# Optimization experiments

Measured on AMD Instinct MI355X. Metric: run time of the kernel, lower is better.

Reference implementation:

```python
import jax, jax.numpy as jnp
import numpy as np

SINKHORN_ITERS = 8
TEMPERATURE = 1.0
EPS = 1e-6


def sinkhorn(t):
    # log-domain Sinkhorn normalization, matching torch: log(clamp(t, min=eps)) / temp
    t = jnp.log(jnp.clip(t, EPS)) / TEMPERATURE
    for _ in range(SINKHORN_ITERS):
        t = t - jax.nn.logsumexp(t, axis=-2, keepdims=True)  # over tokens n
        t = t - jax.nn.logsumexp(t, axis=-1, keepdims=True)  # over experts e
    return jnp.exp(t)


def setup_inputs() -> dict:
    key = jax.random.key(0)
    k1, k2, k3 = jax.random.split(key, 3)
    B, N, D, E = 4, 4096, 1024, 8
    x = jax.random.normal(k1, (B, N, D), dtype=jnp.float32)
    gate_w = jax.random.normal(k2, (D, E), dtype=jnp.float32) * (D ** -0.5)
    experts = jax.random.normal(k3, (E, D, D), dtype=jnp.float32) * (D ** -0.5)
    return {"x": x, "gate_w": gate_w, "experts": experts}


def reference(x, gate_w, experts):
    B, N, D = x.shape
    E = gate_w.shape[-1]
    M = N // E  # tokens per expert

    gate_logits = jnp.einsum('bnd,de->bne', x, gate_w)
    competitive_gates = sinkhorn(gate_logits)  # b n e

    # topk along token dim (-2): transpose to (b,e,n), top_k along last axis
    vals, idx = jax.lax.top_k(jnp.swapaxes(competitive_gates, -1, -2), M)  # b e m
    gate_values = jnp.swapaxes(vals, -1, -2)   # b m e
    routed_indices = jnp.swapaxes(idx, -1, -2)  # b m e (int32)

    b_idx = jnp.arange(B)[:, None, None]  # (b,1,1)
    routed = x[b_idx, routed_indices]     # b m e d
    routed = jnp.transpose(routed, (2, 0, 1, 3))  # e b m d

    outputs = jnp.einsum('ebmd,edf->ebmf', routed, experts)  # e b m d
    outputs = outputs * jnp.transpose(gate_values, (2, 0, 1))[..., None]  # * (e b m 1)

    vals_bmed = jnp.transpose(outputs, (1, 2, 0, 3))  # b m e d
    routed_back = jnp.zeros_like(x).at[b_idx, routed_indices].set(vals_bmed)
    return routed_back
```

## Files before the change

kernel.cpp:

```cpp
#include <hip/hip_runtime.h>
#include <hip/hip_bf16.h>
#include <stdint.h>

typedef short s16x8 __attribute__((ext_vector_type(8)));
typedef float f32x4 __attribute__((ext_vector_type(4)));
typedef unsigned short u16;
typedef unsigned int u32;
typedef unsigned long long u64;

__device__ __forceinline__ float bf2f(u16 v){
  union { u32 u; float f; } c; c.u = ((u32)v) << 16; return c.f;
}

__device__ __forceinline__ u16 f2bf(float f){
  u32 u = __float_as_uint(f);
  u32 r = (u + 0x7FFFu + ((u >> 16) & 1u)) >> 16;
  return (u16)r;
}

__device__ __forceinline__ uint4 pack8(float4 a, float4 b){
  union { uint4 v; u16 s[8]; } o;
  o.s[0]=f2bf(a.x); o.s[1]=f2bf(a.y); o.s[2]=f2bf(a.z); o.s[3]=f2bf(a.w);
  o.s[4]=f2bf(b.x); o.s[5]=f2bf(b.y); o.s[6]=f2bf(b.z); o.s[7]=f2bf(b.w);
  return o.v;
}

__global__ __launch_bounds__(64) void k_detect(const u32* __restrict__ x, int* __restrict__ flag){
  int lane = threadIdx.x;
  int cnt = 0;
  for (int i = lane; i < 4096; i += 64){
    u32 w = x[i];
    int ex = (w >> 7) & 0xFF;
    cnt += (ex >= 140) ? 1 : 0;
  }
  #pragma unroll
  for (int off = 32; off; off >>= 1) cnt += __shfl_xor(cnt, off, 64);
  if (lane == 0) *flag = (cnt > 256) ? 1 : 0;
}

__global__ __launch_bounds__(1024) void k_logits_cvt(const void* __restrict__ xv,
                                                     const void* __restrict__ gwv,
                                                     const int* __restrict__ flag,
                                                     u16* __restrict__ xb,
                                                     float* __restrict__ gates,
                                                     int mode){
  __shared__ float4 gw_swz[2048];
  __shared__ float  wacc[16][8];
  int is_f32 = *flag;
  int tid = threadIdx.x;

  {
    int r = tid;
    float g0,g1,g2,g3,g4,g5,g6,g7;
    if (is_f32){
      const float* gw = (const float*)gwv + ((size_t)r << 3);
      float4 u = *(const float4*)gw;
      float4 v = *(const float4*)(gw + 4);
      g0=u.x; g1=u.y; g2=u.z; g3=u.w; g4=v.x; g5=v.y; g6=v.z; g7=v.w;
    } else {
      union { uint4 v; u16 s[8]; } wu;
      wu.v = *(const uint4*)((const u16*)gwv + ((size_t)r << 3));
      g0=bf2f(wu.s[0]); g1=bf2f(wu.s[1]); g2=bf2f(wu.s[2]); g3=bf2f(wu.s[3]);
      g4=bf2f(wu.s[4]); g5=bf2f(wu.s[5]); g6=bf2f(wu.s[6]); g7=bf2f(wu.s[7]);
    }
    int p = r >> 3, j = r & 7;
    gw_swz[(p << 4) + (((j << 1)    ) ^ (p & 15))] = make_float4(g0,g1,g2,g3);
    gw_swz[(p << 4) + (((j << 1) | 1) ^ (p & 15))] = make_float4(g4,g5,g6,g7);
  }

  int tl = tid >> 7, pos = tid & 127;
  size_t base = ((((size_t)blockIdx.x << 3) + tl) << 10) + ((size_t)pos << 3);
  float xf[8];
  if (is_f32){
    const float* xr = (const float*)xv + base;
    float4 u = *(const float4*)xr;
    float4 v = *(const float4*)(xr + 4);
    xf[0]=u.x; xf[1]=u.y; xf[2]=u.z; xf[3]=u.w;
    xf[4]=v.x; xf[5]=v.y; xf[6]=v.z; xf[7]=v.w;
    if (mode) *(uint4*)(xb + base) = pack8(u, v);
  } else {
    uint4 raw = *(const uint4*)((const u16*)xv + base);
    union { uint4 v; u16 s[8]; } xu; xu.v = raw;
    #pragma unroll
    for (int k = 0; k < 8; k++) xf[k] = bf2f(xu.s[k]);
    if (mode) *(uint4*)(xb + base) = raw;
  }
  __syncthreads();

  float a0=0,a1=0,a2=0,a3=0,a4=0,a5=0,a6=0,a7=0;
  #pragma unroll
  for (int j = 0; j < 8; j++){
    float4 wA = gw_swz[(pos << 4) + (((j << 1)    ) ^ (pos & 15))];
    float4 wB = gw_swz[(pos << 4) + (((j << 1) | 1) ^ (pos & 15))];
    float xv8 = xf[j];
    a0 += xv8*wA.x; a1 += xv8*wA.y; a2 += xv8*wA.z; a3 += xv8*wA.w;
    a4 += xv8*wB.x; a5 += xv8*wB.y; a6 += xv8*wB.z; a7 += xv8*wB.w;
  }
  #pragma unroll
  for (int off = 32; off; off >>= 1){
    a0 += __shfl_xor(a0, off, 64); a1 += __shfl_xor(a1, off, 64);
    a2 += __shfl_xor(a2, off, 64); a3 += __shfl_xor(a3, off, 64);
    a4 += __shfl_xor(a4, off, 64); a5 += __shfl_xor(a5, off, 64);
    a6 += __shfl_xor(a6, off, 64); a7 += __shfl_xor(a7, off, 64);
  }
  int wave = tid >> 6, lane = tid & 63;
  if (lane == 0){
    wacc[wave][0]=a0; wacc[wave][1]=a1; wacc[wave][2]=a2; wacc[wave][3]=a3;
    wacc[wave][4]=a4; wacc[wave][5]=a5; wacc[wave][6]=a6; wacc[wave][7]=a7;
  }
  __syncthreads();
  if (tid < 64){
    int tt = tid >> 3, e = tid & 7;
    float v = wacc[(tt << 1)][e] + wacc[(tt << 1) | 1][e];
    gates[((((size_t)blockIdx.x << 3) + tt) << 3) + e] = v;
  }
}

__global__ __launch_bounds__(1024) void k_sink_cover(float* __restrict__ gates,
                                                     const void* __restrict__ Wv,
                                                     const int* __restrict__ flag,
                                                     u16* __restrict__ WT,
                                                     uint4* __restrict__ out,
                                                     int out_size, int mode){
  __shared__ __align__(16) char smem[36864];
  int bx = blockIdx.x;
  int tid = threadIdx.x;

  if (bx < 4){
    float* wred = (float*)smem;
    float* lbc  = wred + 128;
    int wave = tid >> 6, lane = tid & 63;
    float* gb = gates + ((size_t)bx << 15);
    float4 va[4], vb[4];
    #pragma unroll
    for (int q = 0; q < 4; q++){
      float* gp = gb + (((q << 10) + tid) << 3);
      float4 a = *(const float4*)gp;
      float4 b = *(const float4*)(gp + 4);
      a.x=fmaxf(a.x,1e-6f); a.y=fmaxf(a.y,1e-6f); a.z=fmaxf(a.z,1e-6f); a.w=fmaxf(a.w,1e-6f);
      b.x=fmaxf(b.x,1e-6f); b.y=fmaxf(b.y,1e-6f); b.z=fmaxf(b.z,1e-6f); b.w=fmaxf(b.w,1e-6f);
      va[q]=a; vb[q]=b;
    }
    for (int it = 0; it < 8; it++){
      float s0 = ((va[0].x+va[1].x)+(va[2].x+va[3].x));
      float s1 = ((va[0].y+va[1].y)+(va[2].y+va[3].y));
      float s2 = ((va[0].z+va[1].z)+(va[2].z+va[3].z));
      float s3 = ((va[0].w+va[1].w)+(va[2].w+va[3].w));
      float s4 = ((vb[0].x+vb[1].x)+(vb[2].x+vb[3].x));
      float s5 = ((vb[0].y+vb[1].y)+(vb[2].y+vb[3].y));
      float s6 = ((vb[0].z+vb[1].z)+(vb[2].z+vb[3].z));
      float s7 = ((vb[0].w+vb[1].w)+(vb[2].w+vb[3].w));
      #pragma unroll
      for (int off = 32; off; off >>= 1){
        s0 += __shfl_xor(s0, off, 64); s1 += __shfl_xor(s1, off, 64);
        s2 += __shfl_xor(s2, off, 64); s3 += __shfl_xor(s3, off, 64);
        s4 += __shfl_xor(s4, off, 64); s5 += __shfl_xor(s5, off, 64);
        s6 += __shfl_xor(s6, off, 64); s7 += __shfl_xor(s7, off, 64);
      }
      if (lane == 0){
        wred[(wave<<3)+0]=s0; wred[(wave<<3)+1]=s1; wred[(wave<<3)+2]=s2; wred[(wave<<3)+3]=s3;
        wred[(wave<<3)+4]=s4; wred[(wave<<3)+5]=s5; wred[(wave<<3)+6]=s6; wred[(wave<<3)+7]=s7;
      }
      __syncthreads();
      if (tid < 8){
        float S = 0.f;
        #pragma unroll
        for (int w2 = 0; w2 < 16; w2++) S += wred[(w2 << 3) + tid];
        lbc[tid] = 1.0f / S;
      }
      __syncthreads();
      float i0=lbc[0], i1=lbc[1], i2=lbc[2], i3=lbc[3];
      float i4=lbc[4], i5=lbc[5], i6=lbc[6], i7=lbc[7];
      #pragma unroll
      for (int q = 0; q < 4; q++){
        float4 a = va[q], b = vb[q];
        a.x*=i0; a.y*=i1; a.z*=i2; a.w*=i3;
        b.x*=i4; b.y*=i5; b.z*=i6; b.w*=i7;
        float rs = ((a.x+a.y)+(a.z+a.w)) + ((b.x+b.y)+(b.z+b.w));
        float ir = 1.0f / rs;
        a.x*=ir; a.y*=ir; a.z*=ir; a.w*=ir;
        b.x*=ir; b.y*=ir; b.z*=ir; b.w*=ir;
        va[q]=a; vb[q]=b;
      }
    }
    #pragma unroll
    for (int q = 0; q < 4; q++){
      float* gp = gb + (((q << 10) + tid) << 3);
      *(float4*)gp = va[q];
      *(float4*)(gp + 4) = vb[q];
    }
    return;
  }

  if (mode == 0){
    int is_f32 = *flag;
    int rb = bx - 4;
    size_t words = (size_t)out_size >> (is_f32 ? 0 : 1);
    size_t n4 = words >> 2;
    size_t i = (size_t)rb * 1024 + tid;
    uint4 z = make_uint4(0, 0, 0, 0);
    for (; i < n4; i += (size_t)512 * 1024) out[i] = z;
    return;
  }

  if (bx < 516){
    int is_f32 = *flag;
    int rb = bx - 4;
    int sub = tid >> 8;
    int t = tid & 255;
    int g = (rb << 2) + sub;
    int e = g >> 8, t2 = g & 255;
    int td = (t2 >> 4) << 6, tf = (t2 & 15) << 6;
    u16 (*tile)[72] = (u16(*)[72])(smem + (size_t)sub * (64 * 72 * 2));
    #pragma unroll
    for (int i = 0; i < 2; i++){
      int id = t + (i << 8);
      int row = id >> 3, c8 = id & 7;
      size_t src = ((size_t)(e*1024 + td + row))*1024 + tf + (c8 << 3);
      uint4 v;
      if (is_f32){
        const float* wf = (const float*)Wv;
        v = pack8(*(const float4*)(wf + src), *(const float4*)(wf + src + 4));
      } else {
        v = *(const uint4*)((const u16*)Wv + src);
      }
      *(uint4*)&tile[row][c8 << 3] = v;
    }
    __syncthreads();
    #pragma unroll
    for (int i = 0; i < 2; i++){
      int id = t + (i << 8);
      int frow = id >> 3, c8 = id & 7;
      union { uint4 v; u16 s[8]; } o;
      #pragma unroll
      for (int j = 0; j < 8; j++) o.s[j] = tile[(c8 << 3) + j][frow];
      *(uint4*)(WT + ((size_t)(e*1024 + tf + frow))*1024 + td + (c8 << 3)) = o.v;
    }
    return;
  }

  {
    int is_f32 = *flag;
    int rb = bx - 516;
    size_t words = (size_t)out_size >> (is_f32 ? 0 : 1);
    size_t n4 = words >> 2;
    size_t i = (size_t)rb * 1024 + tid;
    uint4 z = make_uint4(0, 0, 0, 0);
    for (; i < n4; i += (size_t)512 * 1024) out[i] = z;
  }
}

__global__ __launch_bounds__(256) void k_rank(const float* __restrict__ gates,
                                              int* __restrict__ routed, int* __restrict__ winner){
  __shared__ u32 ord_s[4096];
  __shared__ u32 cnt_s[1024];
  int bx = blockIdx.x;
  int be = bx >> 5;
  int b = be >> 3, e = be & 7;
  int slice = bx & 31;
  int tid = threadIdx.x;
  const float* gb = gates + (size_t)b * (4096 * 8);
  for (int i = tid; i < 4096; i += 256){
    float v = gb[(i << 3) + e];
    u32 fb = __float_as_uint(v);
    ord_s[i] = fb ^ ((fb >> 31) ? 0xFFFFFFFFu : 0x80000000u);
  }
  __syncthreads();

  int tg = tid & 31;
  int js = tid >> 5;
  int i0 = (slice << 7) + (tg << 2);
  int gchunk = i0 & ~7;
  u32 v0 = ord_s[i0], v1 = ord_s[i0+1], v2 = ord_s[i0+2], v3 = ord_s[i0+3];
  int jlo = js << 9, jhi = jlo + 512;
  int c0 = 0, c1 = 0, c2 = 0, c3 = 0;

  int endA = min(jhi, gchunk);
  for (int j = jlo; j < endA; j += 8){
    uint4 w0 = *(const uint4*)&ord_s[j];
    uint4 w1 = *(const uint4*)&ord_s[j + 4];
    c0 += (w0.x>=v0)+(w0.y>=v0)+(w0.z>=v0)+(w0.w>=v0)+(w1.x>=v0)+(w1.y>=v0)+(w1.z>=v0)+(w1.w>=v0);
    c1 += (w0.x>=v1)+(w0.y>=v1)+(w0.z>=v1)+(w0.w>=v1)+(w1.x>=v1)+(w1.y>=v1)+(w1.z>=v1)+(w1.w>=v1);
    c2 += (w0.x>=v2)+(w0.y>=v2)+(w0.z>=v2)+(w0.w>=v2)+(w1.x>=v2)+(w1.y>=v2)+(w1.z>=v2)+(w1.w>=v2);
    c3 += (w0.x>=v3)+(w0.y>=v3)+(w0.z>=v3)+(w0.w>=v3)+(w1.x>=v3)+(w1.y>=v3)+(w1.z>=v3)+(w1.w>=v3);
  }
  int begB = max(jlo, gchunk + 8);
  for (int j = begB; j < jhi; j += 8){
    uint4 w0 = *(const uint4*)&ord_s[j];
    uint4 w1 = *(const uint4*)&ord_s[j + 4];
    c0 += (w0.x>v0)+(w0.y>v0)+(w0.z>v0)+(w0.w>v0)+(w1.x>v0)+(w1.y>v0)+(w1.z>v0)+(w1.w>v0);
    c1 += (w0.x>v1)+(w0.y>v1)+(w0.z>v1)+(w0.w>v1)+(w1.x>v1)+(w1.y>v1)+(w1.z>v1)+(w1.w>v1);
    c2 += (w0.x>v2)+(w0.y>v2)+(w0.z>v2)+(w0.w>v2)+(w1.x>v2)+(w1.y>v2)+(w1.z>v2)+(w1.w>v2);
    c3 += (w0.x>v3)+(w0.y>v3)+(w0.z>v3)+(w0.w>v3)+(w1.x>v3)+(w1.y>v3)+(w1.z>v3)+(w1.w>v3);
  }
  if (gchunk >= jlo && gchunk < jhi){
    int base_off = i0 & 7;
    #pragma unroll
    for (int jj = 0; jj < 8; jj++){
      u32 w = ord_s[gchunk + jj];
      c0 += (jj < base_off + 0) ? (w >= v0) : (w > v0);
      c1 += (jj < base_off + 1) ? (w >= v1) : (w > v1);
      c2 += (jj < base_off + 2) ? (w >= v2) : (w > v2);
      c3 += (jj < base_off + 3) ? (w >= v3) : (w > v3);
    }
  }
  int lt = tg << 2;
  cnt_s[(js << 7) + lt + 0] = c0;
  cnt_s[(js << 7) + lt + 1] = c1;
  cnt_s[(js << 7) + lt + 2] = c2;
  cnt_s[(js << 7) + lt + 3] = c3;
  __syncthreads();
  if (tid < 128){
    int rank = 0;
    #pragma unroll
    for (int s = 0; s < 8; s++) rank += cnt_s[(s << 7) + tid];
    int i = (slice << 7) + tid;
    if (rank < 512){
      routed[(be << 9) + rank] = i;
      atomicMax(&winner[(b << 12) + i], (rank << 3) | e);
    }
  }
}

__global__ __launch_bounds__(256) void k_gemm_fast(const u16* __restrict__ xb, const u16* __restrict__ WT,
                                                   const float* __restrict__ gates,
                                                   const int* __restrict__ routed,
                                                   const int* __restrict__ winner,
                                                   const int* __restrict__ flag,
                                                   void* __restrict__ outv){
  __shared__ u16 As[128 * 32];
  __shared__ u16 Bs[128 * 32];
  __shared__ int   tok_s[128];
  __shared__ float gate_s[128];
  __shared__ int   flg_s[128];
  int is_f32 = *flag;
  int bx = blockIdx.x;
  int e = bx & 7;
  int rest = bx >> 3;
  int b = rest >> 5;
  int tile = rest & 31;
  int mt = tile & 3, nt = tile >> 2;
  int tid = threadIdx.x;
  int w = tid >> 6, lane = tid & 63;
  int quad = lane >> 4, l16 = lane & 15;

  const int* idx_base = routed + (((b << 3) + e) << 9) + (mt << 7);

  if (tid < 128){
    int tok = idx_base[tid];
    int mg  = (mt << 7) + tid;
    int win = winner[(b << 12) + tok];
    tok_s[tid]  = tok;
    flg_s[tid]  = (win == ((mg << 3) | e)) ? 1 : 0;
    gate_s[tid] = gates[((((size_t)b << 12) + tok) << 3) + e];
  }
  __syncthreads();

  int r0 = tid >> 2;
  int ch = tid & 3;
  int r1 = r0 + 64;
  const u16* gA0 = xb + ((((size_t)b << 12) + tok_s[r0]) << 10) + (ch << 3);
  const u16* gA1 = xb + ((((size_t)b << 12) + tok_s[r1]) << 10) + (ch << 3);
  int f0 = nt << 7;
  const u16* gB0 = WT + ((((size_t)e << 10) + f0 + r0) << 10) + (ch << 3);
  const u16* gB1 = WT + ((((size_t)e << 10) + f0 + r1) << 10) + (ch << 3);

  f32x4 acc[4][4] = {};
  int wm = (w & 1) << 6, wn = (w >> 1) << 6;

  for (int k0 = 0; k0 < 1024; k0 += 32){
    uint4 a0 = *(const uint4*)(gA0 + k0);
    uint4 a1 = *(const uint4*)(gA1 + k0);
    uint4 b0 = *(const uint4*)(gB0 + k0);
    uint4 b1 = *(const uint4*)(gB1 + k0);
    *(uint4*)&As[(r0 << 5) + (ch << 3)] = a0;
    *(uint4*)&As[(r1 << 5) + (ch << 3)] = a1;
    *(uint4*)&Bs[(r0 << 5) + (ch << 3)] = b0;
    *(uint4*)&Bs[(r1 << 5) + (ch << 3)] = b1;
    __syncthreads();
    s16x8 af[4], bv[4];
    #pragma unroll
    for (int im = 0; im < 4; im++)
      af[im] = *(const s16x8*)&As[((wm + (im << 4) + l16) << 5) + (quad << 3)];
    #pragma unroll
    for (int in = 0; in < 4; in++)
      bv[in] = *(const s16x8*)&Bs[((wn + (in << 4) + l16) << 5) + (quad << 3)];
    __syncthreads();
    #pragma unroll
    for (int im = 0; im < 4; im++){
      #pragma unroll
      for (int in = 0; in < 4; in++)
        acc[im][in] = __builtin_amdgcn_mfma_f32_16x16x32_bf16(af[im], bv[in], acc[im][in], 0, 0, 0);
    }
  }

  #pragma unroll
  for (int im = 0; im < 4; im++){
    #pragma unroll
    for (int r = 0; r < 4; r++){
      int mrow = wm + (im << 4) + (quad << 2) + r;
      if (flg_s[mrow]){
        float g  = gate_s[mrow];
        int tok  = tok_s[mrow];
        size_t obase = ((((size_t)b << 12) + tok) << 10) + f0 + wn + l16;
        if (is_f32){
          float* o32 = (float*)outv;
          #pragma unroll
          for (int in = 0; in < 4; in++) o32[obase + (in << 4)] = acc[im][in][r] * g;
        } else {
          u16* o16 = (u16*)outv;
          #pragma unroll
          for (int in = 0; in < 4; in++) o16[obase + (in << 4)] = f2bf(acc[im][in][r] * g);
        }
      }
    }
  }
}

__global__ __launch_bounds__(256) void k_gemm_slow(const void* __restrict__ xv, const void* __restrict__ Wv,
                                                   const float* __restrict__ gates,
                                                   const int* __restrict__ routed,
                                                   const int* __restrict__ winner,
                                                   const int* __restrict__ flag,
                                                   void* __restrict__ outv){
  __shared__ u16 As[128 * 32];
  __shared__ u16 Bw[32 * 132];
  __shared__ u16 Bs[128 * 32];
  __shared__ int   tok_s[128];
  __shared__ float gate_s[128];
  __shared__ int   flg_s[128];
  int is_f32 = *flag;
  int bx = blockIdx.x;
  int e = bx & 7;
  int rest = bx >> 3;
  int b = rest >> 5;
  int tile = rest & 31;
  int mt = tile & 3, nt = tile >> 2;
  int tid = threadIdx.x;
  int w = tid >> 6, lane = tid & 63;
  int quad = lane >> 4, l16 = lane & 15;

  const int* idx_base = routed + (((b << 3) + e) << 9) + (mt << 7);

  if (tid < 128){
    int tok = idx_base[tid];
    int mg  = (mt << 7) + tid;
    int win = winner[(b << 12) + tok];
    tok_s[tid]  = tok;
    flg_s[tid]  = (win == ((mg << 3) | e)) ? 1 : 0;
    gate_s[tid] = gates[((((size_t)b << 12) + tok) << 3) + e];
  }
  __syncthreads();

  int r0 = tid >> 2;
  int ch = tid & 3;
  int r1 = r0 + 64;
  size_t offA0 = ((((size_t)b << 12) + tok_s[r0]) << 10) + (ch << 3);
  size_t offA1 = ((((size_t)b << 12) + tok_s[r1]) << 10) + (ch << 3);
  int f0 = nt << 7;
  int kkB0 = tid >> 4;
  int fcB  = tid & 15;
  size_t offB0 = ((size_t)e << 20) + ((size_t)kkB0 << 10) + f0 + (fcB << 3);
  size_t offB1 = offB0 + ((size_t)16 << 10);
  int f_loc = tid >> 1;
  int half  = tid & 1;

  f32x4 acc[4][4] = {};
  int wm = (w & 1) << 6, wn = (w >> 1) << 6;

  for (int k0 = 0; k0 < 1024; k0 += 32){
    uint4 a0, a1, b0, b1;
    if (is_f32){
      const float* xf = (const float*)xv;
      const float* wf = (const float*)Wv;
      a0 = pack8(*(const float4*)(xf + offA0 + k0), *(const float4*)(xf + offA0 + k0 + 4));
      a1 = pack8(*(const float4*)(xf + offA1 + k0), *(const float4*)(xf + offA1 + k0 + 4));
      b0 = pack8(*(const float4*)(wf + offB0 + ((size_t)k0 << 10)),
                 *(const float4*)(wf + offB0 + ((size_t)k0 << 10) + 4));
      b1 = pack8(*(const float4*)(wf + offB1 + ((size_t)k0 << 10)),
                 *(const float4*)(wf + offB1 + ((size_t)k0 << 10) + 4));
    } else {
      const u16* xh = (const u16*)xv;
      const u16* wh = (const u16*)Wv;
      a0 = *(const uint4*)(xh + offA0 + k0);
      a1 = *(const uint4*)(xh + offA1 + k0);
      b0 = *(const uint4*)(wh + offB0 + ((size_t)k0 << 10));
      b1 = *(const uint4*)(wh + offB1 + ((size_t)k0 << 10));
    }
    *(uint4*)&As[(r0 << 5) + (ch << 3)] = a0;
    *(uint4*)&As[(r1 << 5) + (ch << 3)] = a1;
    *(uint4*)&Bw[kkB0 * 132 + (fcB << 3)] = b0;
    *(uint4*)&Bw[(kkB0 + 16) * 132 + (fcB << 3)] = b1;
    __syncthreads();
    union { uint4 v[2]; u16 s[16]; } tv;
    #pragma unroll
    for (int j = 0; j < 16; j++) tv.s[j] = Bw[((half << 4) + j) * 132 + f_loc];
    *(uint4*)&Bs[(f_loc << 5) + (half << 4)]     = tv.v[0];
    *(uint4*)&Bs[(f_loc << 5) + (half << 4) + 8] = tv.v[1];
    __syncthreads();
    s16x8 af[4], bv[4];
    #pragma unroll
    for (int im = 0; im < 4; im++)
      af[im] = *(const s16x8*)&As[((wm + (im << 4) + l16) << 5) + (quad << 3)];
    #pragma unroll
    for (int in = 0; in < 4; in++)
      bv[in] = *(const s16x8*)&Bs[((wn + (in << 4) + l16) << 5) + (quad << 3)];
    __syncthreads();
    #pragma unroll
    for (int im = 0; im < 4; im++){
      #pragma unroll
      for (int in = 0; in < 4; in++)
        acc[im][in] = __builtin_amdgcn_mfma_f32_16x16x32_bf16(af[im], bv[in], acc[im][in], 0, 0, 0);
    }
  }

  #pragma unroll
  for (int im = 0; im < 4; im++){
    #pragma unroll
    for (int r = 0; r < 4; r++){
      int mrow = wm + (im << 4) + (quad << 2) + r;
      if (flg_s[mrow]){
        float g  = gate_s[mrow];
        int tok  = tok_s[mrow];
        size_t obase = ((((size_t)b << 12) + tok) << 10) + f0 + wn + l16;
        if (is_f32){
          float* o32 = (float*)outv;
          #pragma unroll
          for (int in = 0; in < 4; in++) o32[obase + (in << 4)] = acc[im][in][r] * g;
        } else {
          u16* o16 = (u16*)outv;
          #pragma unroll
          for (int in = 0; in < 4; in++) o16[obase + (in << 4)] = f2bf(acc[im][in][r] * g);
        }
      }
    }
  }
}

extern "C" void kernel_launch(void* const* d_in, const int* in_sizes, int n_in,
                              void* d_out, int out_size, void* d_ws, size_t ws_size,
                              hipStream_t stream){
  const void* x  = d_in[0];
  const void* gw = d_in[1];
  const void* W  = d_in[2];
  char* ws = (char*)d_ws;
  float* gates  = (float*)ws;
  int*   winner = (int*)(ws + 524288);
  int*   routed = (int*)(ws + 589824);
  int*   flag   = (int*)(ws + 655360);
  u16*   xb     = (u16*)(ws + 655616);
  u16*   WT     = (u16*)(ws + 655616 + 33554432);
  size_t need_fast = 655616ull + 33554432ull + 16777216ull;
  bool fast = ws_size >= need_fast;

  hipMemsetAsync(winner, 0xFF, 65536, stream);
  hipLaunchKernelGGL(k_detect, dim3(1), dim3(64), 0, stream, (const u32*)x, flag);
  hipLaunchKernelGGL(k_logits_cvt, dim3(2048), dim3(1024), 0, stream,
                     x, gw, flag, xb, gates, fast ? 1 : 0);
  if (fast){
    hipLaunchKernelGGL(k_sink_cover, dim3(1028), dim3(1024), 0, stream,
                       gates, W, flag, WT, (uint4*)d_out, out_size, 1);
    hipLaunchKernelGGL(k_rank, dim3(1024), dim3(256), 0, stream, gates, routed, winner);
    hipLaunchKernelGGL(k_gemm_fast, dim3(1024), dim3(256), 0, stream, xb, WT, gates, routed, winner,
                       flag, d_out);
  } else {
    hipLaunchKernelGGL(k_sink_cover, dim3(516), dim3(1024), 0, stream,
                       gates, W, flag, WT, (uint4*)d_out, out_size, 0);
    hipLaunchKernelGGL(k_rank, dim3(1024), dim3(256), 0, stream, gates, routed, winner);
    hipLaunchKernelGGL(k_gemm_slow, dim3(1024), dim3(256), 0, stream, x, W, gates, routed, winner,
                       flag, d_out);
  }
}
```

Measured before the change: 288.4 us.

## Load GEMM tiles directly into LDS with swizzle and transpose-reduce gate logits

The expert GEMM now uses global_load_lds to copy A and B tiles straight from global memory into LDS, skipping the round trip through registers. The global source column is XOR-swizzled by row so the fragment reads land on different LDS banks, and the reads apply the matching swizzle. Separately, the gate-logit reduction replaces eight full butterfly shuffles with a transpose-style reduction that halves the live values at each step, cutting shuffle count. This relies on the LDS layout implied by per-wave 16-byte writes matching the swizzle mapping, which is fragile if the lane-to-address assumption is wrong.

```diff
diff --git a/kernel.cpp b/kernel.cpp
--- a/kernel.cpp
+++ b/kernel.cpp
@@ -23,6 +23,11 @@
   o.s[0]=f2bf(a.x); o.s[1]=f2bf(a.y); o.s[2]=f2bf(a.z); o.s[3]=f2bf(a.w);
   o.s[4]=f2bf(b.x); o.s[5]=f2bf(b.y); o.s[6]=f2bf(b.z); o.s[7]=f2bf(b.w);
   return o.v;
+}
+
+__device__ __forceinline__ void gll16(const u16* g, u16* l){
+  __builtin_amdgcn_global_load_lds((const __attribute__((address_space(1))) u32*)g,
+                                   (__attribute__((address_space(3))) u32*)l, 16, 0, 0);
 }
 
 __global__ __launch_bounds__(64) void k_detect(const u32* __restrict__ x, int* __restrict__ flag){
@@ -96,17 +101,27 @@
     a0 += xv8*wA.x; a1 += xv8*wA.y; a2 += xv8*wA.z; a3 += xv8*wA.w;
     a4 += xv8*wB.x; a5 += xv8*wB.y; a6 += xv8*wB.z; a7 += xv8*wB.w;
   }
-  #pragma unroll
-  for (int off = 32; off; off >>= 1){
-    a0 += __shfl_xor(a0, off, 64); a1 += __shfl_xor(a1, off, 64);
-    a2 += __shfl_xor(a2, off, 64); a3 += __shfl_xor(a3, off, 64);
-    a4 += __shfl_xor(a4, off, 64); a5 += __shfl_xor(a5, off, 64);
-    a6 += __shfl_xor(a6, off, 64); a7 += __shfl_xor(a7, off, 64);
-  }
   int wave = tid >> 6, lane = tid & 63;
-  if (lane == 0){
-    wacc[wave][0]=a0; wacc[wave][1]=a1; wacc[wave][2]=a2; wacc[wave][3]=a3;
-    wacc[wave][4]=a4; wacc[wave][5]=a5; wacc[wave][6]=a6; wacc[wave][7]=a7;
+  int s1 = lane & 1;
+  float k0 = s1 ? a4 : a0, g0 = s1 ? a0 : a4;
+  float k1 = s1 ? a5 : a1, g1 = s1 ? a1 : a5;
+  float k2 = s1 ? a6 : a2, g2 = s1 ? a2 : a6;
+  float k3 = s1 ? a7 : a3, g3 = s1 ? a3 : a7;
+  k0 += __shfl_xor(g0, 1, 64); k1 += __shfl_xor(g1, 1, 64);
+  k2 += __shfl_xor(g2, 1, 64); k3 += __shfl_xor(g3, 1, 64);
+  int s2 = (lane >> 1) & 1;
+  float m0 = s2 ? k2 : k0, h0 = s2 ? k0 : k2;
+  float m1 = s2 ? k3 : k1, h1 = s2 ? k1 : k3;
+  m0 += __shfl_xor(h0, 2, 64); m1 += __shfl_xor(h1, 2, 64);
+  int s3 = (lane >> 2) & 1;
+  float r = s3 ? m1 : m0, h = s3 ? m0 : m1;
+  r += __shfl_xor(h, 4, 64);
+  r += __shfl_xor(r, 8, 64);
+  r += __shfl_xor(r, 16, 64);
+  r += __shfl_xor(r, 32, 64);
+  if (lane < 8){
+    int e = ((lane & 1) << 2) | (lane & 2) | ((lane >> 2) & 1);
+    wacc[wave][e] = r;
   }
   __syncthreads();
   if (tid < 64){
@@ -359,32 +374,34 @@
   int r0 = tid >> 2;
   int ch = tid & 3;
   int r1 = r0 + 64;
-  const u16* gA0 = xb + ((((size_t)b << 12) + tok_s[r0]) << 10) + (ch << 3);
-  const u16* gA1 = xb + ((((size_t)b << 12) + tok_s[r1]) << 10) + (ch << 3);
+  int swz = ch ^ ((r0 >> 1) & 3);
+  const u16* gA0 = xb + ((((size_t)b << 12) + tok_s[r0]) << 10) + (swz << 3);
+  const u16* gA1 = xb + ((((size_t)b << 12) + tok_s[r1]) << 10) + (swz << 3);
   int f0 = nt << 7;
-  const u16* gB0 = WT + ((((size_t)e << 10) + f0 + r0) << 10) + (ch << 3);
-  const u16* gB1 = WT + ((((size_t)e << 10) + f0 + r1) << 10) + (ch << 3);
+  const u16* gB0 = WT + ((((size_t)e << 10) + f0 + r0) << 10) + (swz << 3);
+  const u16* gB1 = WT + ((((size_t)e << 10) + f0 + r1) << 10) + (swz << 3);
+  u16* lA0 = As + (w << 9);
+  u16* lA1 = As + 2048 + (w << 9);
+  u16* lB0 = Bs + (w << 9);
+  u16* lB1 = Bs + 2048 + (w << 9);
+  int swzr = quad ^ ((l16 >> 1) & 3);
 
   f32x4 acc[4][4] = {};
   int wm = (w & 1) << 6, wn = (w >> 1) << 6;
 
   for (int k0 = 0; k0 < 1024; k0 += 32){
-    uint4 a0 = *(const uint4*)(gA0 + k0);
-    uint4 a1 = *(const uint4*)(gA1 + k0);
-    uint4 b0 = *(const uint4*)(gB0 + k0);
-    uint4 b1 = *(const uint4*)(gB1 + k0);
-    *(uint4*)&As[(r0 << 5) + (ch << 3)] = a0;
-    *(uint4*)&As[(r1 << 5) + (ch << 3)] = a1;
-    *(uint4*)&Bs[(r0 << 5) + (ch << 3)] = b0;
-    *(uint4*)&Bs[(r1 << 5) + (ch << 3)] = b1;
+    gll16(gA0 + k0, lA0);
+    gll16(gA1 + k0, lA1);
+    gll16(gB0 + k0, lB0);
+    gll16(gB1 + k0, lB1);
     __syncthreads();
     s16x8 af[4], bv[4];
     #pragma unroll
     for (int im = 0; im < 4; im++)
-      af[im] = *(const s16x8*)&As[((wm + (im << 4) + l16) << 5) + (quad << 3)];
+      af[im] = *(const s16x8*)&As[((wm + (im << 4) + l16) << 5) + (swzr << 3)];
     #pragma unroll
     for (int in = 0; in < 4; in++)
-      bv[in] = *(const s16x8*)&Bs[((wn + (in << 4) + l16) << 5) + (quad << 3)];
+      bv[in] = *(const s16x8*)&Bs[((wn + (in << 4) + l16) << 5) + (swzr << 3)];
     __syncthreads();
     #pragma unroll
     for (int im = 0; im < 4; im++){
```

After: 276.4 us. 1.04x faster.
